# Optimization experiments

Hardware: AMD Instinct MI355X
Metric: run time of the kernel (lower is better)

Reference implementation:

```python
import jax, jax.numpy as jnp
import numpy as np

B, S, E = 4, 2048, 1024
H, D = 16, 64
SCALE = D ** -0.5


def setup_inputs() -> dict:
    key = jax.random.key(0)
    ks = jax.random.split(key, 6)
    x = jax.random.normal(ks[0], (B, S, E), dtype=jnp.float32)
    # per-head projection weights stacked along head axis: [H, E, D]
    Wq = jax.random.normal(ks[1], (H, E, D), dtype=jnp.float32) * 0.02
    Wk = jax.random.normal(ks[2], (H, E, D), dtype=jnp.float32) * 0.02
    Wv = jax.random.normal(ks[3], (H, E, D), dtype=jnp.float32) * 0.02
    # output projection: concat(H*D) -> E, with bias (nn.Linear default)
    Wo = jax.random.normal(ks[4], (H * D, E), dtype=jnp.float32) * 0.02
    bo = jax.random.normal(ks[5], (E,), dtype=jnp.float32) * 0.02
    return {"x": x, "Wq": Wq, "Wk": Wk, "Wv": Wv, "Wo": Wo, "bo": bo}


def reference(x, Wq, Wk, Wv, Wo, bo):
    # batched QKV projections for all heads at once
    q = jnp.einsum('bse,hed->bhsd', x, Wq)
    k = jnp.einsum('bse,hed->bhsd', x, Wk)
    v = jnp.einsum('bse,hed->bhsd', x, Wv)
    # full (non-causal) attention, scores [b,h,s,s]
    scores = jnp.einsum('bhsd,bhtd->bhst', q, k) * SCALE
    attn = jax.nn.softmax(scores, axis=-1)
    o = jnp.einsum('bhst,bhtd->bhsd', attn, v)
    # concat heads in head order along feature dim -> [b,s,H*D]
    o = o.transpose(0, 2, 1, 3).reshape(x.shape[0], x.shape[1], -1)
    return o @ Wo + bo
```

## Files before the change

### kernel.cpp

```cpp
#include <hip/hip_runtime.h>
#include <hip/hip_fp16.h>
#include <stdint.h>

#define BB 4
#define SS 2048
#define EE 1024
#define HH 16
#define DD 64

typedef _Float16 half8 __attribute__((ext_vector_type(8)));
typedef __fp16 fp16x2 __attribute__((ext_vector_type(2)));
typedef float f32x2 __attribute__((ext_vector_type(2)));
typedef float f32x4 __attribute__((ext_vector_type(4)));
typedef float f32x16 __attribute__((ext_vector_type(16)));
typedef uint32_t u32;
typedef uint32_t u32x2 __attribute__((ext_vector_type(2)));

#define MFMA32(a, b, c) __builtin_amdgcn_mfma_f32_16x16x32_f16((a), (b), (c), 0, 0, 0)
#define MFMA3216(a, b, c) __builtin_amdgcn_mfma_f32_32x32x16_f16((a), (b), (c), 0, 0, 0)

#define GLD_LDS16(g, l)                                                        \
  __builtin_amdgcn_global_load_lds(                                            \
      (const __attribute__((address_space(1))) u32*)(const void*)(g),          \
      (__attribute__((address_space(3))) u32*)(void*)(l), 16, 0, 0)

static __device__ __forceinline__ u32 pkh(float a, float b) {
  union { fp16x2 h; u32 u; } z;
  z.h = __builtin_amdgcn_cvt_pkrtz(a, b);
  return z.u;
}

static __device__ __forceinline__ void plswap(u32& a, u32& b) {
  asm("v_permlane32_swap_b32 %0, %1" : "+v"(a), "+v"(b));
}

__global__ __launch_bounds__(256) void conv_x_k(const float* __restrict__ x,
                                                _Float16* __restrict__ xh) {
  size_t i = ((size_t)blockIdx.x * 256 + threadIdx.x) * 8;
  f32x4 a = *(const f32x4*)(x + i);
  f32x4 b = *(const f32x4*)(x + i + 4);
  half8 o;
  o[0] = (_Float16)a[0]; o[1] = (_Float16)a[1];
  o[2] = (_Float16)a[2]; o[3] = (_Float16)a[3];
  o[4] = (_Float16)b[0]; o[5] = (_Float16)b[1];
  o[6] = (_Float16)b[2]; o[7] = (_Float16)b[3];
  *(half8*)(xh + i) = o;
}

__global__ __launch_bounds__(256) void conv_w_k(const float* __restrict__ Wq,
                                                const float* __restrict__ Wk,
                                                const float* __restrict__ Wv,
                                                _Float16* __restrict__ Wt) {
  __shared__ float T[64][65];
  int bid = blockIdx.x;
  int sel = bid >> 8, rem = bid & 255;
  int h = rem >> 4, e0 = (rem & 15) * 64;
  const float* W = (sel == 0 ? Wq : sel == 1 ? Wk : Wv) + (size_t)h * EE * DD;
  float scale = (sel == 0) ? 0.18033688011112042f : 1.0f;
  int tid = threadIdx.x;
  {
    int e = tid >> 2, d0 = (tid & 3) * 16;
#pragma unroll
    for (int i = 0; i < 4; ++i) {
      f32x4 v = *(const f32x4*)(W + (size_t)(e0 + e) * DD + d0 + i * 4);
      T[e][d0 + i * 4 + 0] = v[0];
      T[e][d0 + i * 4 + 1] = v[1];
      T[e][d0 + i * 4 + 2] = v[2];
      T[e][d0 + i * 4 + 3] = v[3];
    }
  }
  __syncthreads();
  {
    int d = tid >> 2, c0 = (tid & 3) * 16;
    half8 o0, o1;
#pragma unroll
    for (int i = 0; i < 8; ++i) o0[i] = (_Float16)(T[c0 + i][d] * scale);
#pragma unroll
    for (int i = 0; i < 8; ++i) o1[i] = (_Float16)(T[c0 + 8 + i][d] * scale);
    _Float16* dst = Wt + ((size_t)sel * 1024 + h * 64 + d) * EE + e0 + c0;
    *(half8*)dst = o0;
    *(half8*)(dst + 8) = o1;
  }
}

__global__ __launch_bounds__(256) void conv_wo_k(const float* __restrict__ Wo,
                                                 _Float16* __restrict__ Wot) {
  __shared__ float T[64][65];
  int bid = blockIdx.x;
  int k0 = (bid >> 4) * 64, n0 = (bid & 15) * 64;
  int tid = threadIdx.x;
  {
    int k = tid >> 2, c0 = (tid & 3) * 16;
#pragma unroll
    for (int i = 0; i < 4; ++i) {
      f32x4 v = *(const f32x4*)(Wo + (size_t)(k0 + k) * EE + n0 + c0 + i * 4);
      T[k][c0 + i * 4 + 0] = v[0];
      T[k][c0 + i * 4 + 1] = v[1];
      T[k][c0 + i * 4 + 2] = v[2];
      T[k][c0 + i * 4 + 3] = v[3];
    }
  }
  __syncthreads();
  {
    int n = tid >> 2, c0 = (tid & 3) * 16;
    half8 o0, o1;
#pragma unroll
    for (int i = 0; i < 8; ++i) o0[i] = (_Float16)T[c0 + i][n];
#pragma unroll
    for (int i = 0; i < 8; ++i) o1[i] = (_Float16)T[c0 + 8 + i][n];
    _Float16* dst = Wot + (size_t)(n0 + n) * EE + k0 + c0;
    *(half8*)dst = o0;
    *(half8*)(dst + 8) = o1;
  }
}

__global__ __launch_bounds__(256) void vtrans_k(const _Float16* __restrict__ v,
                                                _Float16* __restrict__ vT) {
  __shared__ _Float16 T[64][72];
  int bid = blockIdx.x;
  int bh = bid >> 5, st = bid & 31;
  const _Float16* vp = v + (size_t)bh * SS * DD + (size_t)st * 64 * DD;
  _Float16* op = vT + (size_t)bh * DD * SS + (size_t)st * 64;
  int tid = threadIdx.x;
  {
    int r = tid >> 2, c0 = (tid & 3) * 16;
    half8 a = *(const half8*)(vp + (size_t)r * DD + c0);
    half8 b = *(const half8*)(vp + (size_t)r * DD + c0 + 8);
#pragma unroll
    for (int j = 0; j < 8; ++j) T[c0 + j][r] = a[j];
#pragma unroll
    for (int j = 0; j < 8; ++j) T[c0 + 8 + j][r] = b[j];
  }
  __syncthreads();
  {
    int d = tid >> 2, sc = (tid & 3) * 16;
    half8 o0 = *(const half8*)&T[d][sc];
    half8 o1 = *(const half8*)&T[d][sc + 8];
    *(half8*)(op + (size_t)d * SS + sc) = o0;
    *(half8*)(op + (size_t)d * SS + sc + 8) = o1;
  }
}

__global__ __launch_bounds__(256, 3) void qkv_proj_k(
    const _Float16* __restrict__ xh, const _Float16* __restrict__ Wt,
    _Float16* __restrict__ qkv) {
  __shared__ __align__(16) _Float16 As[128 * 32];
  __shared__ __align__(16) _Float16 Bs[128 * 32];
  int bid0 = blockIdx.x;
  int bid = (bid0 & 7) * 192 + (bid0 >> 3);
  int nblk = bid % 24, mblk = bid / 24;
  int row0 = mblk * 128, n0 = nblk * 128;
  int tid = threadIdx.x, lane = tid & 63, w = tid >> 6;
  int wm = w >> 1, wn = w & 1;
  int l15 = lane & 15, lhi = lane >> 4;

  f32x4 acc[4][4];
#pragma unroll
  for (int i = 0; i < 4; ++i)
#pragma unroll
    for (int j = 0; j < 4; ++j) acc[i][j] = (f32x4){0.f, 0.f, 0.f, 0.f};

  const char* Ab = (const char*)xh + (size_t)row0 * 2048;
  const char* Bb = (const char*)Wt + (size_t)n0 * 2048;
  int ob0 = w * 1024 + lane * 16;

  for (int k0 = 0; k0 < EE; k0 += 32) {
    __syncthreads();
    GLD_LDS16(Ab + (size_t)(ob0 >> 6) * 2048 + k0 * 2 + (ob0 & 63),
              (char*)As + w * 1024);
    GLD_LDS16(Ab + (size_t)((ob0 + 4096) >> 6) * 2048 + k0 * 2 + (ob0 & 63),
              (char*)As + 4096 + w * 1024);
    GLD_LDS16(Bb + (size_t)(ob0 >> 6) * 2048 + k0 * 2 + (ob0 & 63),
              (char*)Bs + w * 1024);
    GLD_LDS16(Bb + (size_t)((ob0 + 4096) >> 6) * 2048 + k0 * 2 + (ob0 & 63),
              (char*)Bs + 4096 + w * 1024);
    __syncthreads();
    half8 a[4], b[4];
#pragma unroll
    for (int mf = 0; mf < 4; ++mf)
      a[mf] = *(const half8*)(As + (wm * 64 + mf * 16 + l15) * 32 + 8 * lhi);
#pragma unroll
    for (int nf = 0; nf < 4; ++nf)
      b[nf] = *(const half8*)(Bs + (wn * 64 + nf * 16 + l15) * 32 + 8 * lhi);
#pragma unroll
    for (int mf = 0; mf < 4; ++mf)
#pragma unroll
      for (int nf = 0; nf < 4; ++nf)
        acc[mf][nf] = MFMA32(a[mf], b[nf], acc[mf][nf]);
  }

  const size_t KOFF = (size_t)BB * HH * SS * DD;
#pragma unroll
  for (int mf = 0; mf < 4; ++mf)
#pragma unroll
    for (int nf = 0; nf < 4; ++nf)
#pragma unroll
      for (int r = 0; r < 4; ++r) {
        int row = row0 + wm * 64 + mf * 16 + 4 * lhi + r;
        int n = n0 + wn * 64 + nf * 16 + l15;
        int sel = n >> 10, hh = (n >> 6) & 15, d = n & 63;
        int b_ = row >> 11, s = row & 2047;
        qkv[(size_t)sel * KOFF + (((size_t)b_ * HH + hh) * SS + s) * DD + d] =
            (_Float16)acc[mf][nf][r];
      }
}

__global__ __launch_bounds__(512, 1) void attn_k(
    const _Float16* __restrict__ qkv, const _Float16* __restrict__ vT,
    _Float16* __restrict__ ob) {
  __shared__ __align__(16) _Float16 Ks[2][64 * 64];
  __shared__ __align__(16) _Float16 Vs[2][64 * 64];

  const int bid0 = blockIdx.x;
  const int bid = (bid0 & 7) * 32 + (bid0 >> 3);
  const int bh = bid >> 2, qb = bid & 3;
  const int b_ = bh >> 4, h = bh & 15;
  const size_t KOFF = (size_t)BB * HH * SS * DD;
  const _Float16* qp = qkv + (size_t)bh * SS * DD;
  const char* kp = (const char*)(qkv + KOFF + (size_t)bh * SS * DD);
  const char* vtp = (const char*)(vT + (size_t)bh * DD * SS);

  const int tid = threadIdx.x, lane = tid & 63, w = tid >> 6;
  const int l31 = lane & 31, u = lane >> 5;
  const int q0 = qb * 512 + w * 64;

  half8 qf[4][2];
#pragma unroll
  for (int ekf = 0; ekf < 4; ++ekf)
#pragma unroll
    for (int nq = 0; nq < 2; ++nq)
      qf[ekf][nq] = *(const half8*)(qp +
          (size_t)(q0 + nq * 32 + l31) * DD + ekf * 16 + u * 8);

  f32x16 oa00 = {}, oa10 = {}, oa01 = {}, oa11 = {};
  f32x2 rs2_0 = {0.f, 0.f}, rs2_1 = {0.f, 0.f};

  const int trow = tid >> 3;
  const int scol = ((tid & 7) * 16) ^ (16 * (trow & 7));
  const int lds0 = tid * 16;
  const int xsw = 16 * (l31 & 7);
  const int NT = SS / 64;

  GLD_LDS16(kp + trow * 128 + scol, (char*)Ks[0] + lds0);
  GLD_LDS16(vtp + (size_t)trow * 4096 + scol, (char*)Vs[0] + lds0);
  __syncthreads();

  for (int it = 0; it < NT; ++it) {
    const int cur = it & 1;
    if (it + 1 < NT) {
      GLD_LDS16(kp + (size_t)(it + 1) * 8192 + trow * 128 + scol,
                (char*)Ks[cur ^ 1] + lds0);
      GLD_LDS16(vtp + (size_t)(it + 1) * 128 + (size_t)trow * 4096 + scol,
                (char*)Vs[cur ^ 1] + lds0);
    }
    const char* kb = (const char*)Ks[cur];
    const char* vb = (const char*)Vs[cur];

#pragma unroll
    for (int nt = 0; nt < 2; ++nt) {
      const char* krow = kb + (size_t)(32 * nt + l31) * 128;
      half8 kA0 = *(const half8*)(krow + ((16 * u) ^ xsw));
      half8 kA1 = *(const half8*)(krow + ((32 + 16 * u) ^ xsw));
      half8 kA2 = *(const half8*)(krow + ((64 + 16 * u) ^ xsw));
      half8 kA3 = *(const half8*)(krow + ((96 + 16 * u) ^ xsw));
      f32x16 s0 = {}, s1 = {};
      __builtin_amdgcn_s_setprio(1);
      s0 = MFMA3216(kA0, qf[0][0], s0);
      s1 = MFMA3216(kA0, qf[0][1], s1);
      s0 = MFMA3216(kA1, qf[1][0], s0);
      s1 = MFMA3216(kA1, qf[1][1], s1);
      s0 = MFMA3216(kA2, qf[2][0], s0);
      s1 = MFMA3216(kA2, qf[2][1], s1);
      s0 = MFMA3216(kA3, qf[3][0], s0);
      s1 = MFMA3216(kA3, qf[3][1], s1);
      __builtin_amdgcn_s_setprio(0);

      u32 w0[8], w1[8];
#pragma unroll
      for (int m = 0; m < 8; ++m) {
        float a0 = __builtin_amdgcn_exp2f(s0[2 * m]);
        float a1 = __builtin_amdgcn_exp2f(s0[2 * m + 1]);
        w0[m] = pkh(a0, a1);
        rs2_0 += (f32x2){a0, a1};
        float c0 = __builtin_amdgcn_exp2f(s1[2 * m]);
        float c1 = __builtin_amdgcn_exp2f(s1[2 * m + 1]);
        w1[m] = pkh(c0, c1);
        rs2_1 += (f32x2){c0, c1};
      }

#pragma unroll
      for (int kfl = 0; kfl < 2; ++kfl) {
        u32 p00 = w0[4 * kfl + 0], p02 = w0[4 * kfl + 2];
        u32 p01 = w0[4 * kfl + 1], p03 = w0[4 * kfl + 3];
        plswap(p00, p02);
        plswap(p01, p03);
        u32 p10 = w1[4 * kfl + 0], p12 = w1[4 * kfl + 2];
        u32 p11 = w1[4 * kfl + 1], p13 = w1[4 * kfl + 3];
        plswap(p10, p12);
        plswap(p11, p13);
        union { u32 q[4]; half8 h; } pb0, pb1;
        pb0.q[0] = p00; pb0.q[1] = p01; pb0.q[2] = p02; pb0.q[3] = p03;
        pb1.q[0] = p10; pb1.q[1] = p11; pb1.q[2] = p12; pb1.q[3] = p13;
        const int kf = 2 * nt + kfl;
        const char* vcol = vb + ((32 * kf + 16 * u) ^ xsw);
        half8 vA0 = *(const half8*)(vcol + (size_t)l31 * 128);
        half8 vA1 = *(const half8*)(vcol + (size_t)(32 + l31) * 128);
        __builtin_amdgcn_s_setprio(1);
        oa00 = MFMA3216(vA0, pb0.h, oa00);
        oa10 = MFMA3216(vA1, pb0.h, oa10);
        oa01 = MFMA3216(vA0, pb1.h, oa01);
        oa11 = MFMA3216(vA1, pb1.h, oa11);
        __builtin_amdgcn_s_setprio(0);
      }
    }
    __syncthreads();
  }

  float rs0 = rs2_0.x + rs2_0.y;
  float rs1 = rs2_1.x + rs2_1.y;
  float inv0 = 1.0f / (rs0 + __shfl_xor(rs0, 32, 64));
  float inv1 = 1.0f / (rs1 + __shfl_xor(rs1, 32, 64));

#define STORE_OA(OA, MD, NQ, INV)                                              \
  {                                                                            \
    _Float16* dst = ob + (size_t)(b_ * SS + q0 + 32 * (NQ) + l31) * 1024 +     \
                    h * 64 + 32 * (MD) + 4 * u;                                \
    _Pragma("unroll")                                                          \
    for (int rr = 0; rr < 4; ++rr) {                                           \
      u32x2 pr;                                                                \
      pr.x = pkh(OA[4 * rr + 0] * (INV), OA[4 * rr + 1] * (INV));              \
      pr.y = pkh(OA[4 * rr + 2] * (INV), OA[4 * rr + 3] * (INV));              \
      *(u32x2*)(dst + 8 * rr) = pr;                                            \
    }                                                                          \
  }
  STORE_OA(oa00, 0, 0, inv0)
  STORE_OA(oa10, 1, 0, inv0)
  STORE_OA(oa01, 0, 1, inv1)
  STORE_OA(oa11, 1, 1, inv1)
#undef STORE_OA
}

__global__ __launch_bounds__(256, 3) void oproj_k(
    const _Float16* __restrict__ ob, const _Float16* __restrict__ Wot,
    const float* __restrict__ bo, float* __restrict__ out) {
  __shared__ __align__(16) _Float16 As[128 * 32];
  __shared__ __align__(16) _Float16 Bs[128 * 32];
  int bid0 = blockIdx.x;
  int bid = (bid0 & 7) * 64 + (bid0 >> 3);
  int nblk = bid & 7, mblk = bid >> 3;
  int row0 = mblk * 128, n0 = nblk * 128;
  int tid = threadIdx.x, lane = tid & 63, w = tid >> 6;
  int wm = w >> 1, wn = w & 1;
  int l15 = lane & 15, lhi = lane >> 4;

  f32x4 acc[4][4];
#pragma unroll
  for (int i = 0; i < 4; ++i)
#pragma unroll
    for (int j = 0; j < 4; ++j) acc[i][j] = (f32x4){0.f, 0.f, 0.f, 0.f};

  const char* Ab = (const char*)ob + (size_t)row0 * 2048;
  const char* Bb = (const char*)Wot + (size_t)n0 * 2048;
  int ob0 = w * 1024 + lane * 16;

  for (int k0 = 0; k0 < EE; k0 += 32) {
    __syncthreads();
    GLD_LDS16(Ab + (size_t)(ob0 >> 6) * 2048 + k0 * 2 + (ob0 & 63),
              (char*)As + w * 1024);
    GLD_LDS16(Ab + (size_t)((ob0 + 4096) >> 6) * 2048 + k0 * 2 + (ob0 & 63),
              (char*)As + 4096 + w * 1024);
    GLD_LDS16(Bb + (size_t)(ob0 >> 6) * 2048 + k0 * 2 + (ob0 & 63),
              (char*)Bs + w * 1024);
    GLD_LDS16(Bb + (size_t)((ob0 + 4096) >> 6) * 2048 + k0 * 2 + (ob0 & 63),
              (char*)Bs + 4096 + w * 1024);
    __syncthreads();
    half8 a[4], b[4];
#pragma unroll
    for (int mf = 0; mf < 4; ++mf)
      a[mf] = *(const half8*)(As + (wm * 64 + mf * 16 + l15) * 32 + 8 * lhi);
#pragma unroll
    for (int nf = 0; nf < 4; ++nf)
      b[nf] = *(const half8*)(Bs + (wn * 64 + nf * 16 + l15) * 32 + 8 * lhi);
#pragma unroll
    for (int mf = 0; mf < 4; ++mf)
#pragma unroll
      for (int nf = 0; nf < 4; ++nf)
        acc[mf][nf] = MFMA32(a[mf], b[nf], acc[mf][nf]);
  }

#pragma unroll
  for (int mf = 0; mf < 4; ++mf)
#pragma unroll
    for (int nf = 0; nf < 4; ++nf) {
      int n = n0 + wn * 64 + nf * 16 + l15;
      float bias = bo[n];
#pragma unroll
      for (int r = 0; r < 4; ++r) {
        int row = row0 + wm * 64 + mf * 16 + 4 * lhi + r;
        out[(size_t)row * EE + n] = acc[mf][nf][r] + bias;
      }
    }
}

extern "C" void kernel_launch(void* const* d_in, const int* in_sizes, int n_in,
                              void* d_out, int out_size, void* d_ws, size_t ws_size,
                              hipStream_t stream) {
  const float* x  = (const float*)d_in[0];
  const float* Wq = (const float*)d_in[1];
  const float* Wk = (const float*)d_in[2];
  const float* Wv = (const float*)d_in[3];
  const float* Wo = (const float*)d_in[4];
  const float* bo = (const float*)d_in[5];
  float* out = (float*)d_out;

  const size_t KOFF = (size_t)BB * HH * SS * DD;
  _Float16* qkv = (_Float16*)d_ws;
  _Float16* obuf = qkv + 3 * KOFF;
  _Float16* xh = (_Float16*)d_out;
  _Float16* Wt = xh + (size_t)BB * SS * EE;
  _Float16* vTbuf = xh;
  _Float16* Wot = qkv;

  conv_x_k<<<dim3(4096), dim3(256), 0, stream>>>(x, xh);
  conv_w_k<<<dim3(768), dim3(256), 0, stream>>>(Wq, Wk, Wv, Wt);
  qkv_proj_k<<<dim3(64 * 24), dim3(256), 0, stream>>>(xh, Wt, qkv);
  vtrans_k<<<dim3(64 * 32), dim3(256), 0, stream>>>(qkv + 2 * KOFF, vTbuf);
  attn_k<<<dim3(256), dim3(512), 0, stream>>>(qkv, vTbuf, obuf);
  conv_wo_k<<<dim3(256), dim3(256), 0, stream>>>(Wo, Wot);
  oproj_k<<<dim3(64 * 8), dim3(256), 0, stream>>>(obuf, Wot, bo, out);
}
```

Measured before the change: 196.9 us.

## Software-pipeline QK and PV in attention with 4-deep K buffers and smaller blocks

The attention kernel now runs 256-thread blocks, two per CU, over 512 blocks instead of 512-thread blocks over 256. It keeps four K buffers so K tiles are prefetched two iterations ahead. The loop is skewed so the QK^T MFMAs for the next 32-key sub-tile are issued before the exp/PV work of the current one, which lets MFMA and transcendental/VALU work overlap within a wave. The cost is more registers held live (two score accumulator pairs) and a larger LDS footprint, which could limit occupancy or cause spills.

```diff
diff --git a/kernel.cpp b/kernel.cpp
--- a/kernel.cpp
+++ b/kernel.cpp
@@ -205,15 +205,15 @@
       }
 }
 
-__global__ __launch_bounds__(512, 1) void attn_k(
+__global__ __launch_bounds__(256, 2) void attn_k(
     const _Float16* __restrict__ qkv, const _Float16* __restrict__ vT,
     _Float16* __restrict__ ob) {
-  __shared__ __align__(16) _Float16 Ks[2][64 * 64];
+  __shared__ __align__(16) _Float16 Ks[4][64 * 64];
   __shared__ __align__(16) _Float16 Vs[2][64 * 64];
 
   const int bid0 = blockIdx.x;
-  const int bid = (bid0 & 7) * 32 + (bid0 >> 3);
-  const int bh = bid >> 2, qb = bid & 3;
+  const int bid = (bid0 & 7) * 64 + (bid0 >> 3);
+  const int bh = bid >> 3, qb = bid & 7;
   const int b_ = bh >> 4, h = bh & 15;
   const size_t KOFF = (size_t)BB * HH * SS * DD;
   const _Float16* qp = qkv + (size_t)bh * SS * DD;
@@ -222,7 +222,7 @@
 
   const int tid = threadIdx.x, lane = tid & 63, w = tid >> 6;
   const int l31 = lane & 31, u = lane >> 5;
-  const int q0 = qb * 512 + w * 64;
+  const int q0 = qb * 256 + w * 64;
 
   half8 qf[4][2];
 #pragma unroll
@@ -241,80 +241,104 @@
   const int xsw = 16 * (l31 & 7);
   const int NT = SS / 64;
 
-  GLD_LDS16(kp + trow * 128 + scol, (char*)Ks[0] + lds0);
-  GLD_LDS16(vtp + (size_t)trow * 4096 + scol, (char*)Vs[0] + lds0);
+#define STAGE_K(IT, BUF)                                                       \
+  {                                                                            \
+    const char* s_ = kp + (size_t)(IT) * 8192;                                 \
+    GLD_LDS16(s_ + trow * 128 + scol, (char*)Ks[BUF] + lds0);                  \
+    GLD_LDS16(s_ + (trow + 32) * 128 + scol, (char*)Ks[BUF] + 4096 + lds0);    \
+  }
+#define STAGE_V(IT, BUF)                                                       \
+  {                                                                            \
+    const char* s_ = vtp + (size_t)(IT) * 128;                                 \
+    GLD_LDS16(s_ + (size_t)trow * 4096 + scol, (char*)Vs[BUF] + lds0);         \
+    GLD_LDS16(s_ + (size_t)(trow + 32) * 4096 + scol,                          \
+              (char*)Vs[BUF] + 4096 + lds0);                                   \
+  }
+
+#define QK_SUB(S0, S1, KB, ROFF)                                               \
+  {                                                                            \
+    const char* krow_ = (const char*)(KB) + (size_t)((ROFF) + l31) * 128;      \
+    half8 kA0_ = *(const half8*)(krow_ + ((16 * u) ^ xsw));                    \
+    half8 kA1_ = *(const half8*)(krow_ + ((32 + 16 * u) ^ xsw));               \
+    half8 kA2_ = *(const half8*)(krow_ + ((64 + 16 * u) ^ xsw));               \
+    half8 kA3_ = *(const half8*)(krow_ + ((96 + 16 * u) ^ xsw));               \
+    S0 = (f32x16){};                                                           \
+    S1 = (f32x16){};                                                           \
+    __builtin_amdgcn_s_setprio(1);                                             \
+    S0 = MFMA3216(kA0_, qf[0][0], S0);                                         \
+    S1 = MFMA3216(kA0_, qf[0][1], S1);                                         \
+    S0 = MFMA3216(kA1_, qf[1][0], S0);                                         \
+    S1 = MFMA3216(kA1_, qf[1][1], S1);                                         \
+    S0 = MFMA3216(kA2_, qf[2][0], S0);                                         \
+    S1 = MFMA3216(kA2_, qf[2][1], S1);                                         \
+    S0 = MFMA3216(kA3_, qf[3][0], S0);                                         \
+    S1 = MFMA3216(kA3_, qf[3][1], S1);                                         \
+    __builtin_amdgcn_s_setprio(0);                                             \
+  }
+
+#define FINISH_SUB(S0, S1, NTH, VB)                                            \
+  {                                                                            \
+    u32 w0_[8], w1_[8];                                                        \
+    _Pragma("unroll")                                                          \
+    for (int m = 0; m < 8; ++m) {                                              \
+      float a0_ = __builtin_amdgcn_exp2f(S0[2 * m]);                           \
+      float a1_ = __builtin_amdgcn_exp2f(S0[2 * m + 1]);                       \
+      w0_[m] = pkh(a0_, a1_);                                                  \
+      rs2_0 += (f32x2){a0_, a1_};                                              \
+      float c0_ = __builtin_amdgcn_exp2f(S1[2 * m]);                           \
+      float c1_ = __builtin_amdgcn_exp2f(S1[2 * m + 1]);                       \
+      w1_[m] = pkh(c0_, c1_);                                                  \
+      rs2_1 += (f32x2){c0_, c1_};                                              \
+    }                                                                          \
+    _Pragma("unroll")                                                          \
+    for (int kfl = 0; kfl < 2; ++kfl) {                                        \
+      u32 p00 = w0_[4 * kfl + 0], p02 = w0_[4 * kfl + 2];                      \
+      u32 p01 = w0_[4 * kfl + 1], p03 = w0_[4 * kfl + 3];                      \
+      plswap(p00, p02);                                                        \
+      plswap(p01, p03);                                                        \
+      u32 p10 = w1_[4 * kfl + 0], p12 = w1_[4 * kfl + 2];                      \
+      u32 p11 = w1_[4 * kfl + 1], p13 = w1_[4 * kfl + 3];                      \
+      plswap(p10, p12);                                                        \
+      plswap(p11, p13);                                                        \
+      union { u32 q[4]; half8 h; } pb0, pb1;                                   \
+      pb0.q[0] = p00; pb0.q[1] = p01; pb0.q[2] = p02; pb0.q[3] = p03;          \
+      pb1.q[0] = p10; pb1.q[1] = p11; pb1.q[2] = p12; pb1.q[3] = p13;          \
+      const int kf_ = 2 * (NTH) + kfl;                                         \
+      const char* vcol_ = (const char*)(VB) + ((32 * kf_ + 16 * u) ^ xsw);     \
+      half8 vA0_ = *(const half8*)(vcol_ + (size_t)l31 * 128);                 \
+      half8 vA1_ = *(const half8*)(vcol_ + (size_t)(32 + l31) * 128);          \
+      __builtin_amdgcn_s_setprio(1);                                           \
+      oa00 = MFMA3216(vA0_, pb0.h, oa00);                                      \
+      oa10 = MFMA3216(vA1_, pb0.h, oa10);                                      \
+      oa01 = MFMA3216(vA0_, pb1.h, oa01);                                      \
+      oa11 = MFMA3216(vA1_, pb1.h, oa11);                                      \
+      __builtin_amdgcn_s_setprio(0);                                           \
+    }                                                                          \
+  }
+
+  STAGE_K(0, 0);
+  STAGE_K(1, 1);
+  STAGE_V(0, 0);
   __syncthreads();
 
+  f32x16 SA0, SA1, SB0, SB1;
+  QK_SUB(SA0, SA1, Ks[0], 0);
+
   for (int it = 0; it < NT; ++it) {
-    const int cur = it & 1;
-    if (it + 1 < NT) {
-      GLD_LDS16(kp + (size_t)(it + 1) * 8192 + trow * 128 + scol,
-                (char*)Ks[cur ^ 1] + lds0);
-      GLD_LDS16(vtp + (size_t)(it + 1) * 128 + (size_t)trow * 4096 + scol,
-                (char*)Vs[cur ^ 1] + lds0);
-    }
-    const char* kb = (const char*)Ks[cur];
-    const char* vb = (const char*)Vs[cur];
-
-#pragma unroll
-    for (int nt = 0; nt < 2; ++nt) {
-      const char* krow = kb + (size_t)(32 * nt + l31) * 128;
-      half8 kA0 = *(const half8*)(krow + ((16 * u) ^ xsw));
-      half8 kA1 = *(const half8*)(krow + ((32 + 16 * u) ^ xsw));
-      half8 kA2 = *(const half8*)(krow + ((64 + 16 * u) ^ xsw));
-      half8 kA3 = *(const half8*)(krow + ((96 + 16 * u) ^ xsw));
-      f32x16 s0 = {}, s1 = {};
-      __builtin_amdgcn_s_setprio(1);
-      s0 = MFMA3216(kA0, qf[0][0], s0);
-      s1 = MFMA3216(kA0, qf[0][1], s1);
-      s0 = MFMA3216(kA1, qf[1][0], s0);
-      s1 = MFMA3216(kA1, qf[1][1], s1);
-      s0 = MFMA3216(kA2, qf[2][0], s0);
-      s1 = MFMA3216(kA2, qf[2][1], s1);
-      s0 = MFMA3216(kA3, qf[3][0], s0);
-      s1 = MFMA3216(kA3, qf[3][1], s1);
-      __builtin_amdgcn_s_setprio(0);
-
-      u32 w0[8], w1[8];
-#pragma unroll
-      for (int m = 0; m < 8; ++m) {
-        float a0 = __builtin_amdgcn_exp2f(s0[2 * m]);
-        float a1 = __builtin_amdgcn_exp2f(s0[2 * m + 1]);
-        w0[m] = pkh(a0, a1);
-        rs2_0 += (f32x2){a0, a1};
-        float c0 = __builtin_amdgcn_exp2f(s1[2 * m]);
-        float c1 = __builtin_amdgcn_exp2f(s1[2 * m + 1]);
-        w1[m] = pkh(c0, c1);
-        rs2_1 += (f32x2){c0, c1};
-      }
-
-#pragma unroll
-      for (int kfl = 0; kfl < 2; ++kfl) {
-        u32 p00 = w0[4 * kfl + 0], p02 = w0[4 * kfl + 2];
-        u32 p01 = w0[4 * kfl + 1], p03 = w0[4 * kfl + 3];
-        plswap(p00, p02);
-        plswap(p01, p03);
-        u32 p10 = w1[4 * kfl + 0], p12 = w1[4 * kfl + 2];
-        u32 p11 = w1[4 * kfl + 1], p13 = w1[4 * kfl + 3];
-        plswap(p10, p12);
-        plswap(p11, p13);
-        union { u32 q[4]; half8 h; } pb0, pb1;
-        pb0.q[0] = p00; pb0.q[1] = p01; pb0.q[2] = p02; pb0.q[3] = p03;
-        pb1.q[0] = p10; pb1.q[1] = p11; pb1.q[2] = p12; pb1.q[3] = p13;
-        const int kf = 2 * nt + kfl;
-        const char* vcol = vb + ((32 * kf + 16 * u) ^ xsw);
-        half8 vA0 = *(const half8*)(vcol + (size_t)l31 * 128);
-        half8 vA1 = *(const half8*)(vcol + (size_t)(32 + l31) * 128);
-        __builtin_amdgcn_s_setprio(1);
-        oa00 = MFMA3216(vA0, pb0.h, oa00);
-        oa10 = MFMA3216(vA1, pb0.h, oa10);
-        oa01 = MFMA3216(vA0, pb1.h, oa01);
-        oa11 = MFMA3216(vA1, pb1.h, oa11);
-        __builtin_amdgcn_s_setprio(0);
-      }
-    }
+    const int kcur = it & 3, knext = (it + 1) & 3, kst = (it + 2) & 3;
+    const int vcur = it & 1, vnext = (it + 1) & 1;
+    if (it + 2 < NT) STAGE_K(it + 2, kst);
+    if (it + 1 < NT) STAGE_V(it + 1, vnext);
+    QK_SUB(SB0, SB1, Ks[kcur], 32);
+    FINISH_SUB(SA0, SA1, 0, Vs[vcur]);
+    if (it + 1 < NT) QK_SUB(SA0, SA1, Ks[knext], 0);
+    FINISH_SUB(SB0, SB1, 1, Vs[vcur]);
     __syncthreads();
   }
+#undef STAGE_K
+#undef STAGE_V
+#undef QK_SUB
+#undef FINISH_SUB
 
   float rs0 = rs2_0.x + rs2_0.y;
   float rs1 = rs2_1.x + rs2_1.y;
@@ -425,7 +449,7 @@
   conv_w_k<<<dim3(768), dim3(256), 0, stream>>>(Wq, Wk, Wv, Wt);
   qkv_proj_k<<<dim3(64 * 24), dim3(256), 0, stream>>>(xh, Wt, qkv);
   vtrans_k<<<dim3(64 * 32), dim3(256), 0, stream>>>(qkv + 2 * KOFF, vTbuf);
-  attn_k<<<dim3(256), dim3(512), 0, stream>>>(qkv, vTbuf, obuf);
+  attn_k<<<dim3(512), dim3(256), 0, stream>>>(qkv, vTbuf, obuf);
   conv_wo_k<<<dim3(256), dim3(256), 0, stream>>>(Wo, Wot);
   oproj_k<<<dim3(64 * 8), dim3(256), 0, stream>>>(obuf, Wot, bo, out);
 }
```

Measured after the change: 197.4 us. No clear change (+0.3%).
